# Optimization experiments

Measured on AMD Instinct MI355X. Metric: run time of the kernel, lower is better.

## Reference

```python
import jax, jax.numpy as jnp
import numpy as np

N_NODES = 50000
N_EDGES = 600000
D_IN = 128
D_HID = 128
D_OUT = 40
EPS = 1e-5


def setup_inputs() -> dict:
    key = jax.random.key(0)
    ks = jax.random.split(key, 16)
    inp = {
        "x": jax.random.normal(ks[0], (N_NODES, D_IN), dtype=jnp.float32),
        "edge_index": jax.random.randint(ks[1], (2, N_EDGES), 0, N_NODES, dtype=jnp.int64),
    }
    dims = [(D_IN, D_HID), (D_HID, D_HID), (D_HID, D_OUT)]
    for i, (di, do) in enumerate(dims):
        s = 1.0 / np.sqrt(di)
        inp[f"W_l{i}"] = jax.random.uniform(ks[2 + 3 * i], (di, do), jnp.float32, -s, s)
        inp[f"b_l{i}"] = jax.random.uniform(ks[3 + 3 * i], (do,), jnp.float32, -s, s)
        inp[f"W_r{i}"] = jax.random.uniform(ks[4 + 3 * i], (di, do), jnp.float32, -s, s)
    for i in range(2):  # num_convs - 1 Trans (LayerNorm) blocks
        inp[f"g{i}"] = jnp.ones((D_HID,), jnp.float32)
        inp[f"be{i}"] = jnp.zeros((D_HID,), jnp.float32)
    return inp


def _sage_conv(x, src, dst, W_l, b_l, W_r):
    # mean-aggregate neighbor features at dst, then lin_l(agg) + lin_r(x)
    msg = jax.ops.segment_sum(x[src], dst, num_segments=N_NODES)  # [N, d]
    deg = jax.ops.segment_sum(jnp.ones((src.shape[0],), x.dtype), dst, num_segments=N_NODES)
    agg = msg / jnp.clip(deg, 1.0)[:, None]
    return agg @ W_l + b_l + x @ W_r


def _trans(x, g, b):
    # LayerNorm -> GELU (exact); Dropout p=0 is identity
    mu = jnp.mean(x, axis=-1, keepdims=True)
    var = jnp.mean(jnp.square(x - mu), axis=-1, keepdims=True)
    xn = (x - mu) * jax.lax.rsqrt(var + EPS) * g + b
    return jax.nn.gelu(xn, approximate=False)


def reference(x, edge_index, W_l0, b_l0, W_r0, W_l1, b_l1, W_r1, W_l2, b_l2, W_r2, g0, be0, g1, be1):
    src, dst = edge_index[0], edge_index[1]
    h = _sage_conv(x, src, dst, W_l0, b_l0, W_r0)
    h = _sage_conv(_trans(h, g0, be0), src, dst, W_l1, b_l1, W_r1)
    h = _sage_conv(_trans(h, g1, be1), src, dst, W_l2, b_l2, W_r2)
    return jax.nn.log_softmax(h, axis=1)
```

## Files before the change

### kernel.cpp

```cpp
#include <hip/hip_runtime.h>
#include <math.h>

#define N_NODES 50000
#define N_EDGES 600000
#define DF 128
#define KK 256
#define DOUT 40
#define EPSN 1e-5f
#define NB1 196

typedef __attribute__((ext_vector_type(8))) short sh8;
typedef __attribute__((ext_vector_type(4))) float f32x4;

__device__ __forceinline__ unsigned short f2b(float f) {
  unsigned u = __builtin_bit_cast(unsigned, f);
  unsigned r = u + 0x7FFFu + ((u >> 16) & 1u);
  return (unsigned short)(r >> 16);
}
__device__ __forceinline__ float b2f(unsigned short b) {
  unsigned u = ((unsigned)b) << 16;
  return __builtin_bit_cast(float, u);
}
__device__ __forceinline__ float gelu_f(float x) {
  return 0.5f * x * (1.0f + erff(x * 0.70710678118654752f));
}

__global__ __launch_bounds__(256) void k_count(
    const int* __restrict__ ei, int* __restrict__ counts) {
  int e = blockIdx.x * 256 + threadIdx.x;
  if (e < N_EDGES) atomicAdd(&counts[ei[N_EDGES + e]], 1);
}

__global__ __launch_bounds__(256) void k_bsum(
    const int* __restrict__ counts, int* __restrict__ bsum) {
  int i = blockIdx.x * 256 + threadIdx.x;
  int v = (i < N_NODES) ? counts[i] : 0;
  #pragma unroll
  for (int m = 1; m < 64; m <<= 1) v += __shfl_xor(v, m);
  __shared__ int ws[4];
  if ((threadIdx.x & 63) == 0) ws[threadIdx.x >> 6] = v;
  __syncthreads();
  if (threadIdx.x == 0) bsum[blockIdx.x] = ws[0] + ws[1] + ws[2] + ws[3];
}

__global__ __launch_bounds__(256) void k_bscan(
    const int* __restrict__ bsum, int* __restrict__ bbase) {
  const int t = threadIdx.x, lane = t & 63, w = t >> 6;
  int v = (t < NB1) ? bsum[t] : 0;
  int s = v;
  #pragma unroll
  for (int off = 1; off < 64; off <<= 1) {
    int u = __shfl_up(s, off);
    if (lane >= off) s += u;
  }
  __shared__ int wtot[4];
  if (lane == 63) wtot[w] = s;
  __syncthreads();
  int add = 0;
  for (int k = 0; k < w; ++k) add += wtot[k];
  if (t < NB1) bbase[t] = s + add - v;
}

__global__ __launch_bounds__(256) void k_rowptr(
    const int* __restrict__ counts, const int* __restrict__ bbase,
    int* __restrict__ rowptr, int* __restrict__ cursor,
    float* __restrict__ invdeg) {
  const int i = blockIdx.x * 256 + threadIdx.x;
  const int lane = threadIdx.x & 63, w = threadIdx.x >> 6;
  int c = (i < N_NODES) ? counts[i] : 0;
  int s = c;
  #pragma unroll
  for (int off = 1; off < 64; off <<= 1) {
    int u = __shfl_up(s, off);
    if (lane >= off) s += u;
  }
  __shared__ int wtot[4];
  if (lane == 63) wtot[w] = s;
  __syncthreads();
  int add = bbase[blockIdx.x];
  for (int k = 0; k < w; ++k) add += wtot[k];
  if (i < N_NODES) {
    int excl = s - c + add;
    rowptr[i] = excl;
    cursor[i] = excl;
    invdeg[i] = 1.0f / (float)((c > 1) ? c : 1);
  }
  if (i == 0) rowptr[N_NODES] = N_EDGES;
}

__global__ __launch_bounds__(256) void k_fill(
    const int* __restrict__ ei, int* __restrict__ cursor, int* __restrict__ csr) {
  int e = blockIdx.x * 256 + threadIdx.x;
  if (e < N_EDGES) {
    int d = ei[N_EDGES + e];
    int p = atomicAdd(&cursor[d], 1);
    csr[p] = ei[e];
  }
}

__global__ __launch_bounds__(256) void k_cvt_x(
    const float* __restrict__ x, unsigned* __restrict__ A) {
  int i = blockIdx.x * 256 + threadIdx.x;
  if (i >= N_NODES * 64) return;
  int n = i >> 6, p = i & 63;
  float2 v = ((const float2*)x)[i];
  A[(size_t)n * 128 + 64 + p] = (unsigned)f2b(v.x) | ((unsigned)f2b(v.y) << 16);
}

__global__ __launch_bounds__(256) void k_cvt_w3(
    const float* __restrict__ Wl0, const float* __restrict__ Wr0,
    const float* __restrict__ Wl1, const float* __restrict__ Wr1,
    const float* __restrict__ Wl2, const float* __restrict__ Wr2,
    unsigned short* __restrict__ WT0, unsigned short* __restrict__ WT1,
    unsigned short* __restrict__ WT2b) {
  int i = blockIdx.x * 256 + threadIdx.x;
  if (i >= 75776) return;
  if (i < 65536) {
    const float* Wl; const float* Wr; unsigned short* WT; int j;
    if (i < 32768) { j = i;         Wl = Wl0; Wr = Wr0; WT = WT0; }
    else           { j = i - 32768; Wl = Wl1; Wr = Wr1; WT = WT1; }
    int n = j >> 8, k = j & 255;
    float v = (k < DF) ? Wl[k * DF + n] : Wr[(k - DF) * DF + n];
    WT[j] = f2b(v);
  } else {
    int j = i - 65536;
    int n = j >> 7, k = j & 127;
    float v = (n < DOUT) ? Wl2[k * DOUT + n] : Wr2[k * DOUT + (n - DOUT)];
    WT2b[j] = f2b(v);
  }
}

__global__ __launch_bounds__(256) void k_agg(
    unsigned* __restrict__ A, const int* __restrict__ rowptr,
    const int* __restrict__ csr, const float* __restrict__ invdeg) {
  const int node = (blockIdx.x * 256 + threadIdx.x) >> 6;
  const int lane = threadIdx.x & 63;
  if (node >= N_NODES) return;
  const int beg = rowptr[node], end = rowptr[node + 1];
  float ax = 0.f, ay = 0.f, bx = 0.f, by = 0.f;
  float cx = 0.f, cy = 0.f, dx = 0.f, dy = 0.f;
  int j = beg;
  for (; j + 4 <= end; j += 4) {
    int c0 = csr[j], c1 = csr[j + 1], c2 = csr[j + 2], c3 = csr[j + 3];
    unsigned p0 = A[(size_t)c0 * 128 + 64 + lane];
    unsigned p1 = A[(size_t)c1 * 128 + 64 + lane];
    unsigned p2 = A[(size_t)c2 * 128 + 64 + lane];
    unsigned p3 = A[(size_t)c3 * 128 + 64 + lane];
    ax += b2f((unsigned short)p0); ay += b2f((unsigned short)(p0 >> 16));
    bx += b2f((unsigned short)p1); by += b2f((unsigned short)(p1 >> 16));
    cx += b2f((unsigned short)p2); cy += b2f((unsigned short)(p2 >> 16));
    dx += b2f((unsigned short)p3); dy += b2f((unsigned short)(p3 >> 16));
  }
  for (; j < end; ++j) {
    unsigned p = A[(size_t)csr[j] * 128 + 64 + lane];
    ax += b2f((unsigned short)p); ay += b2f((unsigned short)(p >> 16));
  }
  ax += bx + cx + dx;
  ay += by + cy + dy;
  const float rd = invdeg[node];
  A[(size_t)node * 128 + lane] =
      (unsigned)f2b(ax * rd) | ((unsigned)f2b(ay * rd) << 16);
}

__global__ __launch_bounds__(256) void k_gemm128(
    const unsigned short* __restrict__ Acat, const unsigned short* __restrict__ WT,
    const float* __restrict__ bl, const float* __restrict__ g,
    const float* __restrict__ be, unsigned short* __restrict__ Adst) {
  __shared__ __align__(16) char lds[8704];
  unsigned short* olds = (unsigned short*)lds;
  float2* pp = (float2*)(lds + 8192);

  const int t = threadIdx.x;
  const int rw = blockIdx.x * 16;
  const int wave = t >> 6, lane = t & 63;
  const int lr = lane & 15, lg = lane >> 4;

  #pragma unroll
  for (int it = 0; it < 2; ++it) {
    int id = it * 256 + t;
    int r = id >> 5, c = id & 31;
    sh8 v = *(const sh8*)(Acat + (size_t)(rw + r) * KK + c * 8);
    unsigned off = (unsigned)((r * 512 + c * 16) ^ ((r & 7) << 4));
    *(sh8*)(lds + off) = v;
  }

  sh8 Bfrag[2][8];
  #pragma unroll
  for (int fl = 0; fl < 2; ++fl) {
    const int n = wave * 32 + fl * 16 + lr;
    const sh8* Bp = (const sh8*)(WT + (size_t)n * KK + lg * 8);
    #pragma unroll
    for (int ks = 0; ks < 8; ++ks) Bfrag[fl][ks] = Bp[ks * 4];
  }
  const int col0 = wave * 32 + lr, col1 = col0 + 16;
  const float bc0 = bl[col0], bc1 = bl[col1];
  const float gv0 = g[col0], gv1 = g[col1];
  const float bev0 = be[col0], bev1 = be[col1];

  __syncthreads();

  f32x4 acc0 = {0.f, 0.f, 0.f, 0.f}, acc1 = {0.f, 0.f, 0.f, 0.f};
  #pragma unroll
  for (int ks = 0; ks < 8; ++ks) {
    unsigned off = (unsigned)((lr * 512 + ks * 64 + lg * 16) ^ ((lr & 7) << 4));
    sh8 a = *(const sh8*)(lds + off);
    acc0 = __builtin_amdgcn_mfma_f32_16x16x32_bf16(a, Bfrag[0][ks], acc0, 0, 0, 0);
    acc1 = __builtin_amdgcn_mfma_f32_16x16x32_bf16(a, Bfrag[1][ks], acc1, 0, 0, 0);
  }

  float sv[4], qv[4];
  #pragma unroll
  for (int r = 0; r < 4; ++r) {
    float v0 = acc0[r] + bc0, v1 = acc1[r] + bc1;
    acc0[r] = v0; acc1[r] = v1;
    sv[r] = v0 + v1; qv[r] = v0 * v0 + v1 * v1;
  }
  #pragma unroll
  for (int m = 1; m < 16; m <<= 1) {
    #pragma unroll
    for (int r = 0; r < 4; ++r) {
      sv[r] += __shfl_xor(sv[r], m);
      qv[r] += __shfl_xor(qv[r], m);
    }
  }
  if (lr == 0) {
    #pragma unroll
    for (int r = 0; r < 4; ++r)
      pp[wave * 16 + lg * 4 + r] = make_float2(sv[r], qv[r]);
  }
  __syncthreads();

  #pragma unroll
  for (int r = 0; r < 4; ++r) {
    const int row = lg * 4 + r;
    float2 a0 = pp[row], a1 = pp[16 + row], a2 = pp[32 + row], a3 = pp[48 + row];
    float mu = (a0.x + a1.x + a2.x + a3.x) * (1.0f / 128.0f);
    float var = (a0.y + a1.y + a2.y + a3.y) * (1.0f / 128.0f) - mu * mu;
    float rs = rsqrtf(var + EPSN);
    float xn0 = (acc0[r] - mu) * rs * gv0 + bev0;
    float xn1 = (acc1[r] - mu) * rs * gv1 + bev1;
    olds[row * 136 + col0] = f2b(gelu_f(xn0));
    olds[row * 136 + col1] = f2b(gelu_f(xn1));
  }
  __syncthreads();

  {
    int r = t >> 4, c = t & 15;
    sh8 v = *(const sh8*)((char*)olds + r * 272 + c * 16);
    *(sh8*)(Adst + (size_t)(rw + r) * KK + 128 + c * 8) = v;
  }
}

__global__ __launch_bounds__(256) void k_gemm80(
    const unsigned short* __restrict__ Acat, const unsigned short* __restrict__ WT,
    unsigned short* __restrict__ PQ) {
  __shared__ __align__(16) char lds[16384];
  const int t = threadIdx.x;
  const int rw = blockIdx.x * 64;
  const int wave = t >> 6, lane = t & 63;
  const int lr = lane & 15, lg = lane >> 4;

  #pragma unroll
  for (int it = 0; it < 4; ++it) {
    int id = it * 256 + t;
    int r = id >> 4, c = id & 15;
    int gr = rw + r; if (gr >= N_NODES) gr = N_NODES - 1;
    sh8 v = *(const sh8*)(Acat + (size_t)gr * KK + 128 + c * 8);
    unsigned off = (unsigned)((r * 256 + c * 16) ^ ((r & 7) << 4));
    *(sh8*)(lds + off) = v;
  }

  sh8 Bfrag[5][4];
  #pragma unroll
  for (int f = 0; f < 5; ++f) {
    const int n = f * 16 + lr;
    const sh8* Bp = (const sh8*)(WT + (size_t)n * 128 + lg * 8);
    #pragma unroll
    for (int ks = 0; ks < 4; ++ks) Bfrag[f][ks] = Bp[ks * 4];
  }
  __syncthreads();

  f32x4 accs[5];
  #pragma unroll
  for (int f = 0; f < 5; ++f) accs[f] = (f32x4){0.f, 0.f, 0.f, 0.f};

  #pragma unroll
  for (int ks = 0; ks < 4; ++ks) {
    const int r = wave * 16 + lr;
    unsigned off = (unsigned)((r * 256 + ks * 64 + lg * 16) ^ ((r & 7) << 4));
    sh8 a = *(const sh8*)(lds + off);
    #pragma unroll
    for (int f = 0; f < 5; ++f)
      accs[f] = __builtin_amdgcn_mfma_f32_16x16x32_bf16(a, Bfrag[f][ks], accs[f], 0, 0, 0);
  }
  __syncthreads();

  unsigned short* olds = (unsigned short*)lds;
  #pragma unroll
  for (int f = 0; f < 5; ++f) {
    #pragma unroll
    for (int r = 0; r < 4; ++r) {
      const int row = wave * 16 + lg * 4 + r;
      olds[row * 80 + f * 16 + lr] = f2b(accs[f][r]);
    }
  }
  __syncthreads();

  #pragma unroll
  for (int it = 0; it < 3; ++it) {
    int id = it * 256 + t;
    if (id < 640) {
      int r = (id * 6554) >> 16;
      int c = id - r * 10;
      int gr = rw + r;
      if (gr < N_NODES)
        *(sh8*)(PQ + (size_t)gr * 80 + c * 8) =
            *(const sh8*)((char*)olds + r * 160 + c * 16);
    }
  }
}

__global__ __launch_bounds__(256) void k_final(
    const unsigned short* __restrict__ PQ, const float* __restrict__ bl,
    const int* __restrict__ rowptr, const int* __restrict__ csr,
    const float* __restrict__ invdeg, float* __restrict__ out) {
  const int node = blockIdx.x * 8 + (threadIdx.x >> 5);
  const int hl = threadIdx.x & 31;
  const bool act = (hl < 20);
  const int l = act ? hl : 0;
  const unsigned* Pu = (const unsigned*)PQ;

  const int beg = rowptr[node], end = rowptr[node + 1];
  float ax = 0.f, ay = 0.f, bx = 0.f, by = 0.f;
  float cx = 0.f, cy = 0.f, dx = 0.f, dy = 0.f;
  int j = beg;
  for (; j + 4 <= end; j += 4) {
    int c0 = csr[j], c1 = csr[j + 1], c2 = csr[j + 2], c3 = csr[j + 3];
    unsigned p0 = Pu[(size_t)c0 * 40 + l];
    unsigned p1 = Pu[(size_t)c1 * 40 + l];
    unsigned p2 = Pu[(size_t)c2 * 40 + l];
    unsigned p3 = Pu[(size_t)c3 * 40 + l];
    ax += b2f((unsigned short)p0); ay += b2f((unsigned short)(p0 >> 16));
    bx += b2f((unsigned short)p1); by += b2f((unsigned short)(p1 >> 16));
    cx += b2f((unsigned short)p2); cy += b2f((unsigned short)(p2 >> 16));
    dx += b2f((unsigned short)p3); dy += b2f((unsigned short)(p3 >> 16));
  }
  for (; j < end; ++j) {
    unsigned p = Pu[(size_t)csr[j] * 40 + l];
    ax += b2f((unsigned short)p); ay += b2f((unsigned short)(p >> 16));
  }
  ax += bx + cx + dx;
  ay += by + cy + dy;
  const float rd = invdeg[node];
  unsigned q = Pu[(size_t)node * 40 + 20 + l];
  float v0 = ax * rd + b2f((unsigned short)q) + bl[2 * l];
  float v1 = ay * rd + b2f((unsigned short)(q >> 16)) + bl[2 * l + 1];

  float m = act ? fmaxf(v0, v1) : -INFINITY;
  #pragma unroll
  for (int k = 1; k < 32; k <<= 1) m = fmaxf(m, __shfl_xor(m, k));
  float se = act ? (expf(v0 - m) + expf(v1 - m)) : 0.0f;
  #pragma unroll
  for (int k = 1; k < 32; k <<= 1) se += __shfl_xor(se, k);
  float lse = m + logf(se);
  if (act)
    ((float2*)out)[(size_t)node * 20 + hl] = make_float2(v0 - lse, v1 - lse);
}

extern "C" void kernel_launch(void* const* d_in, const int* in_sizes, int n_in,
                              void* d_out, int out_size, void* d_ws, size_t ws_size,
                              hipStream_t stream) {
  const float* x   = (const float*)d_in[0];
  const int*   ei  = (const int*)d_in[1];
  const float* Wl0 = (const float*)d_in[2];
  const float* bl0 = (const float*)d_in[3];
  const float* Wr0 = (const float*)d_in[4];
  const float* Wl1 = (const float*)d_in[5];
  const float* bl1 = (const float*)d_in[6];
  const float* Wr1 = (const float*)d_in[7];
  const float* Wl2 = (const float*)d_in[8];
  const float* bl2 = (const float*)d_in[9];
  const float* Wr2 = (const float*)d_in[10];
  const float* g0  = (const float*)d_in[11];
  const float* be0 = (const float*)d_in[12];
  const float* g1  = (const float*)d_in[13];
  const float* be1 = (const float*)d_in[14];
  float* out = (float*)d_out;

  unsigned short* A    = (unsigned short*)d_ws;
  unsigned short* PQ   = A + (size_t)N_NODES * KK;
  unsigned short* WT0  = PQ + (size_t)N_NODES * 80;
  unsigned short* WT1  = WT0 + 128 * KK;
  unsigned short* WT2b = WT1 + 128 * KK;
  float* invdeg = (float*)(WT2b + 80 * 128);
  int*   counts = (int*)(invdeg + N_NODES);
  int*   rowptr = counts + N_NODES;
  int*   cursor = rowptr + N_NODES + 1;
  int*   csr    = cursor + N_NODES;
  int*   bsum   = csr + N_EDGES;
  int*   bbase  = bsum + NB1;

  const int egrid = (N_EDGES + 255) / 256;
  const int xgrid = (N_NODES * 64) / 256;
  const int agrid = (N_NODES * 64) / 256;
  const int g128  = N_NODES / 16;
  const int g80   = (N_NODES + 63) / 64;
  const int fgrid = N_NODES / 8;

  hipMemsetAsync(counts, 0, N_NODES * sizeof(int), stream);
  k_count<<<egrid, 256, 0, stream>>>(ei, counts);
  k_bsum<<<NB1, 256, 0, stream>>>(counts, bsum);
  k_bscan<<<1, 256, 0, stream>>>(bsum, bbase);
  k_rowptr<<<NB1, 256, 0, stream>>>(counts, bbase, rowptr, cursor, invdeg);
  k_fill<<<egrid, 256, 0, stream>>>(ei, cursor, csr);

  k_cvt_x<<<xgrid, 256, 0, stream>>>(x, (unsigned*)A);
  k_cvt_w3<<<296, 256, 0, stream>>>(Wl0, Wr0, Wl1, Wr1, Wl2, Wr2, WT0, WT1, WT2b);

  k_agg<<<agrid, 256, 0, stream>>>((unsigned*)A, rowptr, csr, invdeg);
  k_gemm128<<<g128, 256, 0, stream>>>(A, WT0, bl0, g0, be0, A);

  k_agg<<<agrid, 256, 0, stream>>>((unsigned*)A, rowptr, csr, invdeg);
  k_gemm128<<<g128, 256, 0, stream>>>(A, WT1, bl1, g1, be1, A);

  k_gemm80<<<g80, 256, 0, stream>>>(A, WT2b, PQ);
  k_final<<<fgrid, 256, 0, stream>>>(PQ, bl2, rowptr, csr, invdeg, out);
}
```

Baseline: 242.7 us.

## Fuse prep kernels, fold block scan into rowptr, vectorize aggregation with quarter-wave nodes

Merges the edge-count, x-to-bf16 conversion and weight-transpose kernels into one launch selected by block index. It removes the single-block scan kernel: each rowptr block now sums the preceding block totals itself. The aggregation kernel now gives each node 16 lanes that load 16-byte vectors instead of a full wave loading 4-byte words, so each wave handles four nodes. This cuts launch count and gives wider gather loads, at the cost of redundant prefix sums and fewer loads in flight per node.

```diff
diff --git a/kernel.cpp b/kernel.cpp
--- a/kernel.cpp
+++ b/kernel.cpp
@@ -25,10 +25,40 @@
   return 0.5f * x * (1.0f + erff(x * 0.70710678118654752f));
 }
 
-__global__ __launch_bounds__(256) void k_count(
-    const int* __restrict__ ei, int* __restrict__ counts) {
-  int e = blockIdx.x * 256 + threadIdx.x;
-  if (e < N_EDGES) atomicAdd(&counts[ei[N_EDGES + e]], 1);
+__global__ __launch_bounds__(256) void k_prep(
+    const int* __restrict__ ei, int* __restrict__ counts,
+    const float* __restrict__ x, unsigned* __restrict__ A,
+    const float* __restrict__ Wl0, const float* __restrict__ Wr0,
+    const float* __restrict__ Wl1, const float* __restrict__ Wr1,
+    const float* __restrict__ Wl2, const float* __restrict__ Wr2,
+    unsigned short* __restrict__ WT0, unsigned short* __restrict__ WT1,
+    unsigned short* __restrict__ WT2b) {
+  const int b = blockIdx.x, t = threadIdx.x;
+  if (b < 2344) {
+    int e = b * 256 + t;
+    if (e < N_EDGES) atomicAdd(&counts[ei[N_EDGES + e]], 1);
+  } else if (b < 14844) {
+    int i = (b - 2344) * 256 + t;
+    int n = i >> 6, p = i & 63;
+    float2 v = ((const float2*)x)[i];
+    A[(size_t)n * 128 + 64 + p] = (unsigned)f2b(v.x) | ((unsigned)f2b(v.y) << 16);
+  } else {
+    int i = (b - 14844) * 256 + t;
+    if (i >= 75776) return;
+    if (i < 65536) {
+      const float* Wl; const float* Wr; unsigned short* WT; int j;
+      if (i < 32768) { j = i;         Wl = Wl0; Wr = Wr0; WT = WT0; }
+      else           { j = i - 32768; Wl = Wl1; Wr = Wr1; WT = WT1; }
+      int n = j >> 8, k = j & 255;
+      float v = (k < DF) ? Wl[k * DF + n] : Wr[(k - DF) * DF + n];
+      WT[j] = f2b(v);
+    } else {
+      int j = i - 65536;
+      int n = j >> 7, k = j & 127;
+      float v = (n < DOUT) ? Wl2[k * DOUT + n] : Wr2[k * DOUT + (n - DOUT)];
+      WT2b[j] = f2b(v);
+    }
+  }
 }
 
 __global__ __launch_bounds__(256) void k_bsum(
@@ -43,41 +73,31 @@
   if (threadIdx.x == 0) bsum[blockIdx.x] = ws[0] + ws[1] + ws[2] + ws[3];
 }
 
-__global__ __launch_bounds__(256) void k_bscan(
-    const int* __restrict__ bsum, int* __restrict__ bbase) {
-  const int t = threadIdx.x, lane = t & 63, w = t >> 6;
-  int v = (t < NB1) ? bsum[t] : 0;
-  int s = v;
+__global__ __launch_bounds__(256) void k_rowptr(
+    const int* __restrict__ counts, const int* __restrict__ bsum,
+    int* __restrict__ rowptr, int* __restrict__ cursor,
+    float* __restrict__ invdeg) {
+  const int t = threadIdx.x;
+  const int lane = t & 63, w = t >> 6;
+  __shared__ int wtot[4], wpre[4];
+
+  int pre = 0;
+  for (int i = t; i < blockIdx.x; i += 256) pre += bsum[i];
+  #pragma unroll
+  for (int m = 1; m < 64; m <<= 1) pre += __shfl_xor(pre, m);
+  if (lane == 0) wpre[w] = pre;
+
+  const int i = blockIdx.x * 256 + t;
+  int c = (i < N_NODES) ? counts[i] : 0;
+  int s = c;
   #pragma unroll
   for (int off = 1; off < 64; off <<= 1) {
     int u = __shfl_up(s, off);
     if (lane >= off) s += u;
   }
-  __shared__ int wtot[4];
   if (lane == 63) wtot[w] = s;
   __syncthreads();
-  int add = 0;
-  for (int k = 0; k < w; ++k) add += wtot[k];
-  if (t < NB1) bbase[t] = s + add - v;
-}
-
-__global__ __launch_bounds__(256) void k_rowptr(
-    const int* __restrict__ counts, const int* __restrict__ bbase,
-    int* __restrict__ rowptr, int* __restrict__ cursor,
-    float* __restrict__ invdeg) {
-  const int i = blockIdx.x * 256 + threadIdx.x;
-  const int lane = threadIdx.x & 63, w = threadIdx.x >> 6;
-  int c = (i < N_NODES) ? counts[i] : 0;
-  int s = c;
-  #pragma unroll
-  for (int off = 1; off < 64; off <<= 1) {
-    int u = __shfl_up(s, off);
-    if (lane >= off) s += u;
-  }
-  __shared__ int wtot[4];
-  if (lane == 63) wtot[w] = s;
-  __syncthreads();
-  int add = bbase[blockIdx.x];
+  int add = wpre[0] + wpre[1] + wpre[2] + wpre[3];
   for (int k = 0; k < w; ++k) add += wtot[k];
   if (i < N_NODES) {
     int excl = s - c + add;
@@ -85,7 +105,7 @@
     cursor[i] = excl;
     invdeg[i] = 1.0f / (float)((c > 1) ? c : 1);
   }
-  if (i == 0) rowptr[N_NODES] = N_EDGES;
+  if (blockIdx.x == 0 && t == 0) rowptr[N_NODES] = N_EDGES;
 }
 
 __global__ __launch_bounds__(256) void k_fill(
@@ -98,68 +118,47 @@
   }
 }
 
-__global__ __launch_bounds__(256) void k_cvt_x(
-    const float* __restrict__ x, unsigned* __restrict__ A) {
-  int i = blockIdx.x * 256 + threadIdx.x;
-  if (i >= N_NODES * 64) return;
-  int n = i >> 6, p = i & 63;
-  float2 v = ((const float2*)x)[i];
-  A[(size_t)n * 128 + 64 + p] = (unsigned)f2b(v.x) | ((unsigned)f2b(v.y) << 16);
-}
-
-__global__ __launch_bounds__(256) void k_cvt_w3(
-    const float* __restrict__ Wl0, const float* __restrict__ Wr0,
-    const float* __restrict__ Wl1, const float* __restrict__ Wr1,
-    const float* __restrict__ Wl2, const float* __restrict__ Wr2,
-    unsigned short* __restrict__ WT0, unsigned short* __restrict__ WT1,
-    unsigned short* __restrict__ WT2b) {
-  int i = blockIdx.x * 256 + threadIdx.x;
-  if (i >= 75776) return;
-  if (i < 65536) {
-    const float* Wl; const float* Wr; unsigned short* WT; int j;
-    if (i < 32768) { j = i;         Wl = Wl0; Wr = Wr0; WT = WT0; }
-    else           { j = i - 32768; Wl = Wl1; Wr = Wr1; WT = WT1; }
-    int n = j >> 8, k = j & 255;
-    float v = (k < DF) ? Wl[k * DF + n] : Wr[(k - DF) * DF + n];
-    WT[j] = f2b(v);
-  } else {
-    int j = i - 65536;
-    int n = j >> 7, k = j & 127;
-    float v = (n < DOUT) ? Wl2[k * DOUT + n] : Wr2[k * DOUT + (n - DOUT)];
-    WT2b[j] = f2b(v);
-  }
-}
-
 __global__ __launch_bounds__(256) void k_agg(
     unsigned* __restrict__ A, const int* __restrict__ rowptr,
     const int* __restrict__ csr, const float* __restrict__ invdeg) {
-  const int node = (blockIdx.x * 256 + threadIdx.x) >> 6;
+  const int wid = (blockIdx.x * 256 + threadIdx.x) >> 6;
   const int lane = threadIdx.x & 63;
-  if (node >= N_NODES) return;
+  const int sg = lane >> 4, l = lane & 15;
+  const int node = wid * 4 + sg;
   const int beg = rowptr[node], end = rowptr[node + 1];
-  float ax = 0.f, ay = 0.f, bx = 0.f, by = 0.f;
-  float cx = 0.f, cy = 0.f, dx = 0.f, dy = 0.f;
+  const uint4* H4 = (const uint4*)A;
+
+  float f0=0,f1=0,f2=0,f3=0,f4=0,f5=0,f6=0,f7=0;
+  float g0=0,g1=0,g2=0,g3=0,g4=0,g5=0,g6=0,g7=0;
   int j = beg;
-  for (; j + 4 <= end; j += 4) {
-    int c0 = csr[j], c1 = csr[j + 1], c2 = csr[j + 2], c3 = csr[j + 3];
-    unsigned p0 = A[(size_t)c0 * 128 + 64 + lane];
-    unsigned p1 = A[(size_t)c1 * 128 + 64 + lane];
-    unsigned p2 = A[(size_t)c2 * 128 + 64 + lane];
-    unsigned p3 = A[(size_t)c3 * 128 + 64 + lane];
-    ax += b2f((unsigned short)p0); ay += b2f((unsigned short)(p0 >> 16));
-    bx += b2f((unsigned short)p1); by += b2f((unsigned short)(p1 >> 16));
-    cx += b2f((unsigned short)p2); cy += b2f((unsigned short)(p2 >> 16));
-    dx += b2f((unsigned short)p3); dy += b2f((unsigned short)(p3 >> 16));
-  }
-  for (; j < end; ++j) {
-    unsigned p = A[(size_t)csr[j] * 128 + 64 + lane];
-    ax += b2f((unsigned short)p); ay += b2f((unsigned short)(p >> 16));
-  }
-  ax += bx + cx + dx;
-  ay += by + cy + dy;
+  for (; j + 2 <= end; j += 2) {
+    int c0 = csr[j], c1 = csr[j + 1];
+    uint4 p = H4[(size_t)c0 * 32 + 16 + l];
+    uint4 q = H4[(size_t)c1 * 32 + 16 + l];
+    f0 += b2f((unsigned short)p.x); f1 += b2f((unsigned short)(p.x >> 16));
+    f2 += b2f((unsigned short)p.y); f3 += b2f((unsigned short)(p.y >> 16));
+    f4 += b2f((unsigned short)p.z); f5 += b2f((unsigned short)(p.z >> 16));
+    f6 += b2f((unsigned short)p.w); f7 += b2f((unsigned short)(p.w >> 16));
+    g0 += b2f((unsigned short)q.x); g1 += b2f((unsigned short)(q.x >> 16));
+    g2 += b2f((unsigned short)q.y); g3 += b2f((unsigned short)(q.y >> 16));
+    g4 += b2f((unsigned short)q.z); g5 += b2f((unsigned short)(q.z >> 16));
+    g6 += b2f((unsigned short)q.w); g7 += b2f((unsigned short)(q.w >> 16));
+  }
+  if (j < end) {
+    uint4 p = H4[(size_t)csr[j] * 32 + 16 + l];
+    f0 += b2f((unsigned short)p.x); f1 += b2f((unsigned short)(p.x >> 16));
+    f2 += b2f((unsigned short)p.y); f3 += b2f((unsigned short)(p.y >> 16));
+    f4 += b2f((unsigned short)p.z); f5 += b2f((unsigned short)(p.z >> 16));
+    f6 += b2f((unsigned short)p.w); f7 += b2f((unsigned short)(p.w >> 16));
+  }
+  f0+=g0; f1+=g1; f2+=g2; f3+=g3; f4+=g4; f5+=g5; f6+=g6; f7+=g7;
   const float rd = invdeg[node];
-  A[(size_t)node * 128 + lane] =
-      (unsigned)f2b(ax * rd) | ((unsigned)f2b(ay * rd) << 16);
+  uint4 o;
+  o.x = (unsigned)f2b(f0 * rd) | ((unsigned)f2b(f1 * rd) << 16);
+  o.y = (unsigned)f2b(f2 * rd) | ((unsigned)f2b(f3 * rd) << 16);
+  o.z = (unsigned)f2b(f4 * rd) | ((unsigned)f2b(f5 * rd) << 16);
+  o.w = (unsigned)f2b(f6 * rd) | ((unsigned)f2b(f7 * rd) << 16);
+  ((uint4*)A)[(size_t)node * 32 + l] = o;
 }
 
 __global__ __launch_bounds__(256) void k_gemm128(
@@ -398,24 +397,21 @@
   int*   cursor = rowptr + N_NODES + 1;
   int*   csr    = cursor + N_NODES;
   int*   bsum   = csr + N_EDGES;
-  int*   bbase  = bsum + NB1;
 
   const int egrid = (N_EDGES + 255) / 256;
-  const int xgrid = (N_NODES * 64) / 256;
-  const int agrid = (N_NODES * 64) / 256;
+  const int pgrid = 2344 + 12500 + 296;
+  const int agrid = N_NODES / 16;
   const int g128  = N_NODES / 16;
   const int g80   = (N_NODES + 63) / 64;
   const int fgrid = N_NODES / 8;
 
   hipMemsetAsync(counts, 0, N_NODES * sizeof(int), stream);
-  k_count<<<egrid, 256, 0, stream>>>(ei, counts);
+  k_prep<<<pgrid, 256, 0, stream>>>(ei, counts, x, (unsigned*)A,
+                                    Wl0, Wr0, Wl1, Wr1, Wl2, Wr2,
+                                    WT0, WT1, WT2b);
   k_bsum<<<NB1, 256, 0, stream>>>(counts, bsum);
-  k_bscan<<<1, 256, 0, stream>>>(bsum, bbase);
-  k_rowptr<<<NB1, 256, 0, stream>>>(counts, bbase, rowptr, cursor, invdeg);
+  k_rowptr<<<NB1, 256, 0, stream>>>(counts, bsum, rowptr, cursor, invdeg);
   k_fill<<<egrid, 256, 0, stream>>>(ei, cursor, csr);
-
-  k_cvt_x<<<xgrid, 256, 0, stream>>>(x, (unsigned*)A);
-  k_cvt_w3<<<296, 256, 0, stream>>>(Wl0, Wr0, Wl1, Wr1, Wl2, Wr2, WT0, WT1, WT2b);
 
   k_agg<<<agrid, 256, 0, stream>>>((unsigned*)A, rowptr, csr, invdeg);
   k_gemm128<<<g128, 256, 0, stream>>>(A, WT0, bl0, g0, be0, A);
```

After: 223.8 us. 7.8% less time.
